# Kernel optimization log

Measured on AMD Instinct MI355X. Metric: run time of the kernel, lower is better.

The kernel has to match this reference:

```python
import jax, jax.numpy as jnp
import numpy as np

TOP_K = 8
N_EXPERTS = 64
ALPHA = 0.01

def setup_inputs() -> dict:
    key = jax.random.key(0)
    k1, k2 = jax.random.split(key)
    hidden_states = jax.random.normal(k1, (8, 4096, 1024), dtype=jnp.float32)
    weight = jax.random.normal(k2, (N_EXPERTS, 1024), dtype=jnp.float32) * 0.02
    return {"hidden_states": hidden_states, "weight": weight}

def reference(hidden_states, weight):
    bsz, seq_len, h = hidden_states.shape
    tokens = hidden_states.reshape(-1, h).astype(jnp.float32)          # [T, h]
    logits = tokens @ weight.astype(jnp.float32).T                     # [T, E]
    scores = jax.nn.softmax(logits, axis=-1)                           # [T, E]
    topk_weights, topk_indices = jax.lax.top_k(scores, TOP_K)          # [T, K]
    topk_indices = jnp.clip(topk_indices, 0, N_EXPERTS - 1)
    # renormalize top-k probabilities (norm_topk_prob=True, top_k>1)
    denom = topk_weights.sum(axis=-1, keepdims=True) + 1e-20
    topk_weights = topk_weights / denom
    # expert usage counts (bincount / scatter path)
    expert_counts = jnp.zeros((N_EXPERTS,), jnp.int32).at[topk_indices.reshape(-1)].add(1)
    # sequence aux loss (training path, seq_aux=True)
    idx_b = topk_indices.reshape(bsz, seq_len * TOP_K)                 # [B, S*K]
    ce = jnp.zeros((bsz, N_EXPERTS), jnp.float32)
    ce = ce.at[jnp.arange(bsz)[:, None], idx_b].add(1.0)
    ce = ce * (N_EXPERTS / (seq_len * TOP_K))
    scores_seq = scores.reshape(bsz, seq_len, N_EXPERTS)
    aux_loss = ((ce * scores_seq.mean(axis=1)).sum(axis=1)).mean() * ALPHA
    return (topk_indices.astype(jnp.int32),
            topk_weights.astype(hidden_states.dtype),
            aux_loss,
            expert_counts)
```

## Files before the change

### kernel.cpp

```cpp
#include <hip/hip_runtime.h>

#define NTOK 32768
#define HDIM 1024
#define NEXP 64
#define TK   8
#define NB   8
#define SEQ  4096

#define MB   64
#define KC   64
#define NTHR 256

typedef __attribute__((ext_vector_type(8))) short bf16x8;
typedef __attribute__((ext_vector_type(4))) float f32x4;

union BF8 { bf16x8 v; unsigned u[4]; };

__device__ inline unsigned f2bf(float x) {
    unsigned u = __float_as_uint(x);
    return (u + 0x7FFFu + ((u >> 16) & 1u)) >> 16;
}

__device__ inline void split4(float4 v, unsigned* hp, unsigned* lp) {
    unsigned h0 = f2bf(v.x), h1 = f2bf(v.y), h2 = f2bf(v.z), h3 = f2bf(v.w);
    unsigned l0 = f2bf(v.x - __uint_as_float(h0 << 16));
    unsigned l1 = f2bf(v.y - __uint_as_float(h1 << 16));
    unsigned l2 = f2bf(v.z - __uint_as_float(h2 << 16));
    unsigned l3 = f2bf(v.w - __uint_as_float(h3 << 16));
    hp[0] = h0 | (h1 << 16); hp[1] = h2 | (h3 << 16);
    lp[0] = l0 | (l1 << 16); lp[1] = l2 | (l3 << 16);
}

__device__ __forceinline__ void gl16(const void* g, void* l) {
    __builtin_amdgcn_global_load_lds(
        (const __attribute__((address_space(1))) void*)g,
        (__attribute__((address_space(3))) void*)l, 16, 0, 0);
}

__global__ void wsplit(const float* __restrict__ w,
                       unsigned short* __restrict__ whi,
                       unsigned short* __restrict__ wlo)
{
    int idx = blockIdx.x * 256 + threadIdx.x;
    float4 v = ((const float4*)w)[idx];
    unsigned hp[2], lp[2];
    split4(v, hp, lp);
    ((uint2*)whi)[idx] = make_uint2(hp[0], hp[1]);
    ((uint2*)wlo)[idx] = make_uint2(lp[0], lp[1]);
}

__global__ __launch_bounds__(NTHR, 2) void moe_main(
    const float* __restrict__ hidden,
    const unsigned short* __restrict__ whi,
    const unsigned short* __restrict__ wlo,
    float* __restrict__ out,
    float* __restrict__ ws)
{
    __shared__ __align__(16) unsigned char smem[32768];
    float*          sA  = (float*)smem;
    unsigned short* sBh = (unsigned short*)(smem + 16384);
    unsigned short* sBl = (unsigned short*)(smem + 24576);
    float*          sLog = (float*)smem;
    __shared__ float smSum[NEXP];
    __shared__ int   hist[NEXP];

    const int tid   = threadIdx.x;
    const int w     = tid >> 6;
    const int l     = tid & 63;
    const int m     = l & 15;
    const int quad  = l >> 4;
    const int t0    = blockIdx.x * MB;
    const int wbase = tid & 192;

    if (tid < NEXP) { smSum[tid] = 0.f; hist[tid] = 0; }

    f32x4 acc[4];
#pragma unroll
    for (int n = 0; n < 4; ++n) acc[n] = (f32x4)0.f;

    for (int c = 0; c < HDIM / KC; ++c) {
        const int kc = c * KC;
        __syncthreads();
#pragma unroll
        for (int i = 0; i < 4; ++i) {
            int sl = i * 256 + tid;
            int cc = sl >> 6, r = sl & 63;
            gl16(hidden + (size_t)(t0 + r) * HDIM + kc + cc * 4,
                 smem + (size_t)(i * 256 + wbase) * 16);
        }
#pragma unroll
        for (int i = 0; i < 2; ++i) {
            int sl = i * 256 + tid;
            int cc = sl >> 6, r = sl & 63;
            gl16(whi + (size_t)r * HDIM + kc + cc * 8,
                 smem + 16384 + (size_t)(i * 256 + wbase) * 16);
            gl16(wlo + (size_t)r * HDIM + kc + cc * 8,
                 smem + 24576 + (size_t)(i * 256 + wbase) * 16);
        }
        __syncthreads();

#pragma unroll
        for (int s = 0; s < 2; ++s) {
            const int c0 = 8 * s + 2 * quad;
            const int ar = w * 16 + m;
            float4 a0 = *(const float4*)&sA[c0 * 256 + ar * 4];
            float4 a1 = *(const float4*)&sA[(c0 + 1) * 256 + ar * 4];
            BF8 ah, al;
            split4(a0, &ah.u[0], &al.u[0]);
            split4(a1, &ah.u[2], &al.u[2]);
            const int cb = 4 * s + quad;
#pragma unroll
            for (int n = 0; n < 4; ++n) {
                const int br = n * 16 + m;
                bf16x8 bh = *(const bf16x8*)&sBh[cb * 512 + br * 8];
                bf16x8 bl = *(const bf16x8*)&sBl[cb * 512 + br * 8];
                acc[n] = __builtin_amdgcn_mfma_f32_16x16x32_bf16(ah.v, bh, acc[n], 0, 0, 0);
                acc[n] = __builtin_amdgcn_mfma_f32_16x16x32_bf16(al.v, bh, acc[n], 0, 0, 0);
                acc[n] = __builtin_amdgcn_mfma_f32_16x16x32_bf16(ah.v, bl, acc[n], 0, 0, 0);
            }
        }
    }

    __syncthreads();
#pragma unroll
    for (int n = 0; n < 4; ++n)
#pragma unroll
        for (int r = 0; r < 4; ++r)
            sLog[(w * 16 + quad * 4 + r) * 66 + n * 16 + m] = acc[n][r];
    __syncthreads();

    float regSm = 0.f;
    for (int j = 0; j < 16; ++j) {
        int tt = w * 16 + j;
        float x = sLog[tt * 66 + l];
        double xd = (double)x;
        float mx = x;
#pragma unroll
        for (int off = 32; off; off >>= 1) mx = fmaxf(mx, __shfl_xor(mx, off));
        float p = __expf(x - mx);
        float sden = p;
#pragma unroll
        for (int off = 32; off; off >>= 1) sden += __shfl_xor(sden, off);
        float score = p / sden;
        regSm += score;

        double vd = xd;
        int selIdx = 0; float selVal = 0.f;
#pragma unroll
        for (int r = 0; r < TK; ++r) {
            unsigned long long u = (unsigned long long)__double_as_longlong(vd);
            unsigned long long mk = (u & 0x8000000000000000ull) ? ~u : (u | 0x8000000000000000ull);
            unsigned long long key = (mk & 0xFFFFFFFFFFFFFFC0ull) | (unsigned long long)(63 - l);
#pragma unroll
            for (int off = 32; off; off >>= 1) {
                unsigned long long o = __shfl_xor(key, off);
                if (o > key) key = o;
            }
            int winner = 63 - (int)(key & 63ull);
            float wsc = __shfl(score, winner);
            if (l == r) { selIdx = winner; selVal = wsc; }
            if (l == winner) vd = -__builtin_inf();
        }
        float dv = (l < TK) ? selVal : 0.f;
#pragma unroll
        for (int off = 32; off; off >>= 1) dv += __shfl_xor(dv, off);
        int t = t0 + tt;
        if (l < TK) {
            out[(size_t)t * TK + l] = (float)selIdx;
            out[(size_t)NTOK * TK + (size_t)t * TK + l] = selVal / (dv + 1e-20f);
            atomicAdd(&hist[selIdx], 1);
        }
    }
    atomicAdd(&smSum[l], regSm);
    __syncthreads();
    if (tid < NEXP) {
        int b = blockIdx.x >> 6;
        atomicAdd(&ws[b * NEXP + tid], (float)hist[tid]);
        atomicAdd(&ws[NB * NEXP + b * NEXP + tid], smSum[tid]);
    }
}

__global__ void moe_finalize(const float* __restrict__ ws, float* __restrict__ out)
{
    int e = threadIdx.x;
    float cnt = 0.f, accv = 0.f;
#pragma unroll
    for (int b = 0; b < NB; ++b) {
        float c  = ws[b * NEXP + e];
        float sm = ws[NB * NEXP + b * NEXP + e];
        cnt += c;
        accv += c * sm;
    }
    out[(size_t)NTOK * TK * 2 + 1 + e] = cnt;
#pragma unroll
    for (int off = 32; off; off >>= 1) accv += __shfl_xor(accv, off);
    if (e == 0) {
        float aux = 0.01f * accv * ((float)NEXP / ((float)SEQ * (float)TK))
                    / (float)SEQ / (float)NB;
        out[(size_t)NTOK * TK * 2] = aux;
    }
}

extern "C" void kernel_launch(void* const* d_in, const int* in_sizes, int n_in,
                              void* d_out, int out_size, void* d_ws, size_t ws_size,
                              hipStream_t stream)
{
    const float* hidden = (const float*)d_in[0];
    const float* weight = (const float*)d_in[1];
    float* out  = (float*)d_out;
    float* wsf  = (float*)d_ws;
    unsigned short* whi = (unsigned short*)(wsf + 2 * NB * NEXP);
    unsigned short* wlo = whi + NEXP * HDIM;

    hipMemsetAsync(d_ws, 0, 2 * NB * NEXP * sizeof(float), stream);
    wsplit<<<64, 256, 0, stream>>>(weight, whi, wlo);
    moe_main<<<NTOK / MB, NTHR, 0, stream>>>(hidden, whi, wlo, out, wsf);
    moe_finalize<<<1, 64, 0, stream>>>(wsf, out);
}
```

Before: 262.7 us.

## Double-buffer hidden tiles, pre-swizzle weights to fragment layout, per-thread top-k

Weights are now pre-split into bf16 hi/lo in MFMA-fragment order so each lane loads its B fragments straight from global memory instead of staging them through LDS. Hidden tiles are double-buffered with an XOR swizzle, and each wave now covers 32 rows with 128 threads per block. The wave-wide shuffle top-k is replaced by a per-thread insertion sort over the 64 logits. Top-k weights are recomputed from the logits and the row max. This removes one barrier per chunk and the shuffle-heavy selection, but it adds register pressure and leaves the top-k on a single wave.

```diff
diff --git a/kernel.cpp b/kernel.cpp
--- a/kernel.cpp
+++ b/kernel.cpp
@@ -9,7 +9,8 @@
 
 #define MB   64
 #define KC   64
-#define NTHR 256
+#define NCH  (HDIM / KC)
+#define NTHR 128
 
 typedef __attribute__((ext_vector_type(8))) short bf16x8;
 typedef __attribute__((ext_vector_type(4))) float f32x4;
@@ -41,26 +42,31 @@
                        unsigned short* __restrict__ whi,
                        unsigned short* __restrict__ wlo)
 {
-    int idx = blockIdx.x * 256 + threadIdx.x;
-    float4 v = ((const float4*)w)[idx];
-    unsigned hp[2], lp[2];
-    split4(v, hp, lp);
-    ((uint2*)whi)[idx] = make_uint2(hp[0], hp[1]);
-    ((uint2*)wlo)[idx] = make_uint2(lp[0], lp[1]);
+    int T = blockIdx.x * 256 + threadIdx.x;
+    int slot = T >> 6, l = T & 63;
+    int c = slot >> 3, s = (slot >> 2) & 1, n = slot & 3;
+    int e = n * 16 + (l & 15);
+    int k = c * 64 + s * 32 + (l >> 4) * 8;
+    const float* src = w + (size_t)e * HDIM + k;
+    float4 v0 = *(const float4*)(src);
+    float4 v1 = *(const float4*)(src + 4);
+    unsigned hp[4], lp[4];
+    split4(v0, &hp[0], &lp[0]);
+    split4(v1, &hp[2], &lp[2]);
+    ((uint4*)whi)[T] = make_uint4(hp[0], hp[1], hp[2], hp[3]);
+    ((uint4*)wlo)[T] = make_uint4(lp[0], lp[1], lp[2], lp[3]);
 }
 
 __global__ __launch_bounds__(NTHR, 2) void moe_main(
     const float* __restrict__ hidden,
-    const unsigned short* __restrict__ whi,
-    const unsigned short* __restrict__ wlo,
+    const unsigned short* __restrict__ w2hi,
+    const unsigned short* __restrict__ w2lo,
     float* __restrict__ out,
     float* __restrict__ ws)
 {
     __shared__ __align__(16) unsigned char smem[32768];
-    float*          sA  = (float*)smem;
-    unsigned short* sBh = (unsigned short*)(smem + 16384);
-    unsigned short* sBl = (unsigned short*)(smem + 24576);
-    float*          sLog = (float*)smem;
+    float* sLog = (float*)smem;
+    __shared__ float mxArr[MB];
     __shared__ float smSum[NEXP];
     __shared__ int   hist[NEXP];
 
@@ -68,111 +74,147 @@
     const int w     = tid >> 6;
     const int l     = tid & 63;
     const int m     = l & 15;
-    const int quad  = l >> 4;
+    const int q     = l >> 4;
     const int t0    = blockIdx.x * MB;
-    const int wbase = tid & 192;
+    const int wbase = tid & 64;
 
     if (tid < NEXP) { smSum[tid] = 0.f; hist[tid] = 0; }
 
-    f32x4 acc[4];
-#pragma unroll
-    for (int n = 0; n < 4; ++n) acc[n] = (f32x4)0.f;
-
-    for (int c = 0; c < HDIM / KC; ++c) {
-        const int kc = c * KC;
+    f32x4 acc[2][4];
+#pragma unroll
+    for (int mt = 0; mt < 2; ++mt)
+#pragma unroll
+        for (int n = 0; n < 4; ++n) acc[mt][n] = (f32x4)0.f;
+
+#pragma unroll
+    for (int i = 0; i < 8; ++i) {
+        int slot = i * NTHR + tid;
+        int r = slot >> 4, p = slot & 15, b = p ^ (r & 15);
+        gl16(hidden + (size_t)(t0 + r) * HDIM + b * 4,
+             smem + (size_t)(i * NTHR + wbase) * 16);
+    }
+    __syncthreads();
+
+    for (int c = 0; c < NCH; ++c) {
+        const unsigned char* Ab = smem + (c & 1) * 16384;
+
+        bf16x8 bh[2][4], bl[2][4];
+#pragma unroll
+        for (int s = 0; s < 2; ++s)
+#pragma unroll
+            for (int n = 0; n < 4; ++n) {
+                size_t off = ((size_t)(c * 8 + s * 4 + n) * 64 + l) * 8;
+                bh[s][n] = *(const bf16x8*)(w2hi + off);
+                bl[s][n] = *(const bf16x8*)(w2lo + off);
+            }
+
+        if (c + 1 < NCH) {
+            unsigned char* nb = smem + ((c + 1) & 1) * 16384;
+            const int kc = (c + 1) * KC;
+#pragma unroll
+            for (int i = 0; i < 8; ++i) {
+                int slot = i * NTHR + tid;
+                int r = slot >> 4, p = slot & 15, b = p ^ (r & 15);
+                gl16(hidden + (size_t)(t0 + r) * HDIM + kc + b * 4,
+                     nb + (size_t)(i * NTHR + wbase) * 16);
+            }
+        }
+
+#pragma unroll
+        for (int s = 0; s < 2; ++s) {
+            BF8 ah[2], al[2];
+#pragma unroll
+            for (int mt = 0; mt < 2; ++mt) {
+                int r = w * 32 + mt * 16 + m;
+                int b0 = s * 8 + q * 2;
+                int p0 = b0 ^ (r & 15), p1 = (b0 + 1) ^ (r & 15);
+                float4 a0 = *(const float4*)(Ab + ((size_t)r * 16 + p0) * 16);
+                float4 a1 = *(const float4*)(Ab + ((size_t)r * 16 + p1) * 16);
+                split4(a0, &ah[mt].u[0], &al[mt].u[0]);
+                split4(a1, &ah[mt].u[2], &al[mt].u[2]);
+            }
+#pragma unroll
+            for (int n = 0; n < 4; ++n)
+#pragma unroll
+                for (int mt = 0; mt < 2; ++mt) {
+                    acc[mt][n] = __builtin_amdgcn_mfma_f32_16x16x32_bf16(ah[mt].v, bh[s][n], acc[mt][n], 0, 0, 0);
+                    acc[mt][n] = __builtin_amdgcn_mfma_f32_16x16x32_bf16(al[mt].v, bh[s][n], acc[mt][n], 0, 0, 0);
+                    acc[mt][n] = __builtin_amdgcn_mfma_f32_16x16x32_bf16(ah[mt].v, bl[s][n], acc[mt][n], 0, 0, 0);
+                }
+        }
         __syncthreads();
-#pragma unroll
-        for (int i = 0; i < 4; ++i) {
-            int sl = i * 256 + tid;
-            int cc = sl >> 6, r = sl & 63;
-            gl16(hidden + (size_t)(t0 + r) * HDIM + kc + cc * 4,
-                 smem + (size_t)(i * 256 + wbase) * 16);
-        }
-#pragma unroll
-        for (int i = 0; i < 2; ++i) {
-            int sl = i * 256 + tid;
-            int cc = sl >> 6, r = sl & 63;
-            gl16(whi + (size_t)r * HDIM + kc + cc * 8,
-                 smem + 16384 + (size_t)(i * 256 + wbase) * 16);
-            gl16(wlo + (size_t)r * HDIM + kc + cc * 8,
-                 smem + 24576 + (size_t)(i * 256 + wbase) * 16);
-        }
-        __syncthreads();
-
-#pragma unroll
-        for (int s = 0; s < 2; ++s) {
-            const int c0 = 8 * s + 2 * quad;
-            const int ar = w * 16 + m;
-            float4 a0 = *(const float4*)&sA[c0 * 256 + ar * 4];
-            float4 a1 = *(const float4*)&sA[(c0 + 1) * 256 + ar * 4];
-            BF8 ah, al;
-            split4(a0, &ah.u[0], &al.u[0]);
-            split4(a1, &ah.u[2], &al.u[2]);
-            const int cb = 4 * s + quad;
-#pragma unroll
-            for (int n = 0; n < 4; ++n) {
-                const int br = n * 16 + m;
-                bf16x8 bh = *(const bf16x8*)&sBh[cb * 512 + br * 8];
-                bf16x8 bl = *(const bf16x8*)&sBl[cb * 512 + br * 8];
-                acc[n] = __builtin_amdgcn_mfma_f32_16x16x32_bf16(ah.v, bh, acc[n], 0, 0, 0);
-                acc[n] = __builtin_amdgcn_mfma_f32_16x16x32_bf16(al.v, bh, acc[n], 0, 0, 0);
-                acc[n] = __builtin_amdgcn_mfma_f32_16x16x32_bf16(ah.v, bl, acc[n], 0, 0, 0);
-            }
-        }
-    }
-
-    __syncthreads();
-#pragma unroll
-    for (int n = 0; n < 4; ++n)
-#pragma unroll
-        for (int r = 0; r < 4; ++r)
-            sLog[(w * 16 + quad * 4 + r) * 66 + n * 16 + m] = acc[n][r];
+    }
+
+#pragma unroll
+    for (int mt = 0; mt < 2; ++mt)
+#pragma unroll
+        for (int n = 0; n < 4; ++n)
+#pragma unroll
+            for (int r = 0; r < 4; ++r)
+                sLog[(w * 32 + mt * 16 + q * 4 + r) * 66 + n * 16 + m] = acc[mt][n][r];
     __syncthreads();
 
     float regSm = 0.f;
-    for (int j = 0; j < 16; ++j) {
-        int tt = w * 16 + j;
-        float x = sLog[tt * 66 + l];
-        double xd = (double)x;
+    for (int j = 0; j < 32; ++j) {
+        int t = w * 32 + j;
+        float x = sLog[t * 66 + l];
         float mx = x;
 #pragma unroll
         for (int off = 32; off; off >>= 1) mx = fmaxf(mx, __shfl_xor(mx, off));
         float p = __expf(x - mx);
-        float sden = p;
-#pragma unroll
-        for (int off = 32; off; off >>= 1) sden += __shfl_xor(sden, off);
-        float score = p / sden;
-        regSm += score;
-
-        double vd = xd;
-        int selIdx = 0; float selVal = 0.f;
-#pragma unroll
-        for (int r = 0; r < TK; ++r) {
-            unsigned long long u = (unsigned long long)__double_as_longlong(vd);
-            unsigned long long mk = (u & 0x8000000000000000ull) ? ~u : (u | 0x8000000000000000ull);
-            unsigned long long key = (mk & 0xFFFFFFFFFFFFFFC0ull) | (unsigned long long)(63 - l);
-#pragma unroll
-            for (int off = 32; off; off >>= 1) {
-                unsigned long long o = __shfl_xor(key, off);
-                if (o > key) key = o;
-            }
-            int winner = 63 - (int)(key & 63ull);
-            float wsc = __shfl(score, winner);
-            if (l == r) { selIdx = winner; selVal = wsc; }
-            if (l == winner) vd = -__builtin_inf();
-        }
-        float dv = (l < TK) ? selVal : 0.f;
-#pragma unroll
-        for (int off = 32; off; off >>= 1) dv += __shfl_xor(dv, off);
-        int t = t0 + tt;
-        if (l < TK) {
-            out[(size_t)t * TK + l] = (float)selIdx;
-            out[(size_t)NTOK * TK + (size_t)t * TK + l] = selVal / (dv + 1e-20f);
-            atomicAdd(&hist[selIdx], 1);
-        }
+        float sd = p;
+#pragma unroll
+        for (int off = 32; off; off >>= 1) sd += __shfl_xor(sd, off);
+        regSm += p / sd;
+        if (l == 0) mxArr[t] = mx;
     }
     atomicAdd(&smSum[l], regSm);
     __syncthreads();
+
+    if (w == 0) {
+        const float mx = mxArr[l];
+        unsigned long long s8[TK];
+#pragma unroll
+        for (int j = 0; j < TK; ++j) s8[j] = 0ull;
+        for (int e = 0; e < NEXP; ++e) {
+            float x = sLog[l * 66 + e];
+            unsigned u = __float_as_uint(x);
+            unsigned k32 = (u & 0x80000000u) ? ~u : (u | 0x80000000u);
+            unsigned long long key = ((unsigned long long)k32 << 6)
+                                   | (unsigned long long)(63 - e);
+            if (key > s8[TK - 1]) {
+#pragma unroll
+                for (int j = 0; j < TK; ++j) {
+                    unsigned long long hi = s8[j] > key ? s8[j] : key;
+                    key = s8[j] > key ? key : s8[j];
+                    s8[j] = hi;
+                }
+            }
+        }
+        float ev[TK]; int ei[TK]; float sum = 0.f;
+#pragma unroll
+        for (int j = 0; j < TK; ++j) {
+            unsigned k32 = (unsigned)(s8[j] >> 6);
+            unsigned u = (k32 >> 31) ? (k32 ^ 0x80000000u) : ~k32;
+            ev[j] = __expf(__uint_as_float(u) - mx);
+            sum += ev[j];
+            ei[j] = 63 - (int)(s8[j] & 63ull);
+        }
+        int t = t0 + l;
+        float4 i0 = make_float4((float)ei[0], (float)ei[1], (float)ei[2], (float)ei[3]);
+        float4 i1 = make_float4((float)ei[4], (float)ei[5], (float)ei[6], (float)ei[7]);
+        *(float4*)(out + (size_t)t * TK)     = i0;
+        *(float4*)(out + (size_t)t * TK + 4) = i1;
+        float rs = 1.f / (sum + 1e-20f);
+        float4 w0 = make_float4(ev[0] * rs, ev[1] * rs, ev[2] * rs, ev[3] * rs);
+        float4 w1 = make_float4(ev[4] * rs, ev[5] * rs, ev[6] * rs, ev[7] * rs);
+        *(float4*)(out + (size_t)NTOK * TK + (size_t)t * TK)     = w0;
+        *(float4*)(out + (size_t)NTOK * TK + (size_t)t * TK + 4) = w1;
+#pragma unroll
+        for (int j = 0; j < TK; ++j) atomicAdd(&hist[ei[j]], 1);
+    }
+    __syncthreads();
+
     if (tid < NEXP) {
         int b = blockIdx.x >> 6;
         atomicAdd(&ws[b * NEXP + tid], (float)hist[tid]);
@@ -209,11 +251,11 @@
     const float* weight = (const float*)d_in[1];
     float* out  = (float*)d_out;
     float* wsf  = (float*)d_ws;
-    unsigned short* whi = (unsigned short*)(wsf + 2 * NB * NEXP);
-    unsigned short* wlo = whi + NEXP * HDIM;
+    unsigned short* w2hi = (unsigned short*)(wsf + 2 * NB * NEXP);
+    unsigned short* w2lo = w2hi + NEXP * HDIM;
 
     hipMemsetAsync(d_ws, 0, 2 * NB * NEXP * sizeof(float), stream);
-    wsplit<<<64, 256, 0, stream>>>(weight, whi, wlo);
-    moe_main<<<NTOK / MB, NTHR, 0, stream>>>(hidden, whi, wlo, out, wsf);
+    wsplit<<<32, 256, 0, stream>>>(weight, w2hi, w2lo);
+    moe_main<<<NTOK / MB, NTHR, 0, stream>>>(hidden, w2hi, w2lo, out, wsf);
     moe_finalize<<<1, 64, 0, stream>>>(wsf, out);
 }
```

Measured after the change: 237.5 us. 1.11x faster.
